# Optimization experiments

Measured on AMD Instinct MI355X. Metric: run time of the kernel, lower is better.

## Reference

```python
import jax, jax.numpy as jnp
import numpy as np

N_NODES = 50000
E_TRAIN = 800000
E_POS = 200000
E_NEG = 200000
F_IN = 128


def gcn_conv(x, W, b, src, dst, n):
    """PyG-style GCNConv: add self-loops, symmetric deg^{-1/2} norm, linear, scatter-add."""
    loop = jnp.arange(n, dtype=src.dtype)
    s = jnp.concatenate([src, loop])  # [E+N]
    d = jnp.concatenate([dst, loop])
    deg = jax.ops.segment_sum(jnp.ones(d.shape, dtype=x.dtype), d, num_segments=n)
    dis = jax.lax.rsqrt(jnp.maximum(deg, 1.0))  # deg >= 1 due to self-loops
    norm = dis[s] * dis[d]  # [E+N]
    h = x @ W  # [N, out]
    msg = h[s] * norm[:, None]  # gather + per-edge scale
    return jax.ops.segment_sum(msg, d, num_segments=n) + b


def reference(x, train_pos_edge_index, pos_edge_index, neg_edge_index, W1, b1, W2, b2, W3, b3):
    src, dst = train_pos_edge_index[0], train_pos_edge_index[1]
    h = jax.nn.relu(gcn_conv(x, W1, b1, src, dst, N_NODES))
    h = jax.nn.relu(gcn_conv(h, W2, b2, src, dst, N_NODES))
    h = gcn_conv(h, W3, b3, src, dst, N_NODES)
    te = jnp.concatenate([pos_edge_index, neg_edge_index], axis=-1)  # [2, E_pos+E_neg]
    x_j = h[te[0]]
    x_i = h[te[1]]
    return jnp.einsum('ef,ef->e', x_i, x_j)


def setup_inputs() -> dict:
    key = jax.random.key(0)
    ks = jax.random.split(key, 10)
    glorot = lambda k, fi, fo: jax.random.normal(k, (fi, fo), dtype=jnp.float32) * np.float32(np.sqrt(2.0 / (fi + fo)))
    return {
        'x': jax.random.normal(ks[0], (N_NODES, F_IN), dtype=jnp.float32),
        'train_pos_edge_index': jax.random.randint(ks[1], (2, E_TRAIN), 0, N_NODES, dtype=jnp.int32),
        'pos_edge_index': jax.random.randint(ks[2], (2, E_POS), 0, N_NODES, dtype=jnp.int32),
        'neg_edge_index': jax.random.randint(ks[3], (2, E_NEG), 0, N_NODES, dtype=jnp.int32),
        'W1': glorot(ks[4], F_IN, 256), 'b1': jnp.zeros((256,), jnp.float32),
        'W2': glorot(ks[5], 256, 128), 'b2': jnp.zeros((128,), jnp.float32),
        'W3': glorot(ks[6], 128, 64), 'b3': jnp.zeros((64,), jnp.float32),
    }
```

## Files before the change

### kernel.cpp

```cpp
#include <hip/hip_runtime.h>
#include <math.h>

#define N_NODES 50000
#define E_TRAIN 800000
#define E_POS 200000
#define E_NEG 200000

#define NBUCK 196
#define BSTRIDE 5120
#define PSTRIDE 9216
#define PARTA_BLOCKS 196


__device__ inline void split_bf16(float f, short& h, short& l) {
    unsigned u = __float_as_uint(f);
    h = (short)(u >> 16);
    float rem = f - __uint_as_float(u & 0xFFFF0000u);
    l = (short)(__float_as_uint(rem) >> 16);
}

__device__ inline unsigned short f2bf_rne(float f) {
    unsigned u = __float_as_uint(f);
    unsigned r = u + 0x7FFFu + ((u >> 16) & 1u);
    return (unsigned short)(r >> 16);
}

__device__ inline float bf2f(unsigned short h) {
    return __uint_as_float(((unsigned)h) << 16);
}

#define WTOT (128 * 256 + 256 * 128 + 128 * 64)


__global__ void partA_prep_kernel(
        const int* __restrict__ src, const int* __restrict__ dst,
        int* __restrict__ gcount, unsigned int* __restrict__ temp, int e,
        const float* __restrict__ W1, short* __restrict__ W1h, short* __restrict__ W1l,
        const float* __restrict__ W2, short* __restrict__ W2h, short* __restrict__ W2l,
        const float* __restrict__ W3, short* __restrict__ W3h, short* __restrict__ W3l,
        const float* __restrict__ x, unsigned short* __restrict__ xb, int n4) {
    __shared__ int hist[NBUCK];
    __shared__ int base[NBUCK];
    __shared__ int lcur[NBUCK];
    int tid = threadIdx.x;
    if (blockIdx.x < PARTA_BLOCKS) {
        for (int i = tid; i < NBUCK; i += 256) hist[i] = 0;
        __syncthreads();
        int start = blockIdx.x * 4096;
        int stop = min(start + 4096, e);
        for (int i = start + tid; i < stop; i += 256)
            atomicAdd(&hist[dst[i] >> 8], 1);
        __syncthreads();
        for (int i = tid; i < NBUCK; i += 256) {
            base[i] = atomicAdd(&gcount[i], hist[i]);
            lcur[i] = 0;
        }
        __syncthreads();
        for (int i = start + tid; i < stop; i += 256) {
            int d = dst[i];
            int b = d >> 8;
            int off = atomicAdd(&lcur[b], 1);
            temp[(size_t)b * BSTRIDE + base[b] + off] = ((unsigned)src[i] << 8) | (unsigned)(d & 255);
        }
    } else {
        int i = (blockIdx.x - PARTA_BLOCKS) * 256 + tid;
        if (i < WTOT) {
            const float* W; short *Wh, *Wl; int K, N;
            if (i < 128 * 256) { W = W1; Wh = W1h; Wl = W1l; K = 128; N = 256; }
            else if (i < 128 * 256 + 256 * 128) { i -= 128 * 256; W = W2; Wh = W2h; Wl = W2l; K = 256; N = 128; }
            else { i -= 128 * 256 + 256 * 128; W = W3; Wh = W3h; Wl = W3l; K = 128; N = 64; }
            int k = i / N, n = i - k * N;
            short h, l;
            split_bf16(W[i], h, l);
            Wh[(size_t)n * K + k] = h;
            Wl[(size_t)n * K + k] = l;
        } else {
            int j = i - WTOT;
            if (j < n4) {
                float4 v = ((const float4*)x)[j];
                ushort4 o;
                o.x = f2bf_rne(v.x); o.y = f2bf_rne(v.y);
                o.z = f2bf_rne(v.z); o.w = f2bf_rne(v.w);
                ((ushort4*)xb)[j] = o;
            }
        }
    }
}


__global__ void partB_kernel(const unsigned int* __restrict__ temp,
                             const int* __restrict__ gcount,
                             float* __restrict__ dis, int* __restrict__ offs, int* __restrict__ ends,
                             unsigned short* __restrict__ csr) {
    __shared__ int cnt[256];
    __shared__ int loc[256];
    __shared__ int cursor[256];
    int b = blockIdx.x;
    int t = threadIdx.x;
    int total = gcount[b];
    size_t tbase = (size_t)b * BSTRIDE;
    cnt[t] = 0;
    __syncthreads();
    for (int i = t; i < total; i += 256)
        atomicAdd(&cnt[temp[tbase + i] & 255], 1);
    __syncthreads();
    int c = cnt[t];
    int pc = (c + 15) & ~15;
    loc[t] = pc;
    __syncthreads();
    for (int d = 1; d < 256; d <<= 1) {
        int u = 0;
        if (t >= d) u = loc[t - d];
        __syncthreads();
        if (t >= d) loc[t] += u;
        __syncthreads();
    }
    int excl = loc[t] - pc;
    int node = b * 256 + t;
    int gstart = b * PSTRIDE + excl;
    if (node < N_NODES) {
        dis[node] = 1.0f / sqrtf((float)(c + 1));
        offs[node] = gstart;
        ends[node] = gstart + pc;
    }
    cursor[t] = gstart;
    __syncthreads();
    for (int i = t; i < total; i += 256) {
        unsigned v = temp[tbase + i];
        int pos = atomicAdd(&cursor[v & 255], 1);
        csr[pos] = (unsigned short)(v >> 8);
    }
    __syncthreads();
    for (int j = c; j < pc; j++)
        csr[gstart + j] = 0xFFFFu;
}

__global__ void wdis_kernel(unsigned short* __restrict__ csr,
                            const float* __restrict__ dis,
                            float* __restrict__ wdis, int n) {
    int i = blockIdx.x * blockDim.x + threadIdx.x;
    if (i < n) {
        unsigned short s = csr[i];
        if (s == 0xFFFFu) { csr[i] = 0; wdis[i] = 0.f; }
        else wdis[i] = dis[s];
    }
}


typedef short bf16x8 __attribute__((ext_vector_type(8)));
typedef float f32x4 __attribute__((ext_vector_type(4)));

template<int BN, bool BR, bool OBF>
__global__ __launch_bounds__(512) void gemm_fulln_kernel(
        const float* __restrict__ A,
        const short* __restrict__ Bth, const short* __restrict__ Btl,
        const float* __restrict__ bias, float* __restrict__ C,
        unsigned short* __restrict__ Cb,
        int M, int K) {
    constexpr int NI = BN / 16;
    constexpr int BCH = BN * 4;
    constexpr int BP = (BCH + 511) / 512;
    constexpr size_t BSZ = (size_t)2 * BN * 40 * 2;
    constexpr size_t TSZ = (size_t)8 * 16 * 68 * 4;
    __shared__ __align__(16) char smem[BSZ > TSZ ? BSZ : TSZ];
    short* Bhi = (short*)smem;
    short* Blo = (short*)(smem + (size_t)BN * 40 * 2);
    float* tr  = (float*)smem;

    int tid = threadIdx.x;
    int lane = tid & 63;
    int wv = tid >> 6;
    int brow = blockIdx.x * 128;
    int m_lane = lane & 15;
    int kgrp = lane >> 4;

    int myrow = brow + wv * 16 + m_lane;
    if (myrow >= M) myrow = M - 1;
    const float* Ap = &A[(size_t)myrow * K + kgrp * 8];

    f32x4 acc[NI];
    #pragma unroll
    for (int i = 0; i < NI; i++) acc[i] = (f32x4){0.f, 0.f, 0.f, 0.f};

    int4 bhReg[BP], blReg[BP];
    float4 aN0, aN1, aC0, aC1;

    auto loadB = [&](int k0) {
        #pragma unroll
        for (int p = 0; p < BP; p++) {
            int idx = p * 512 + tid;
            if (idx < BCH) {
                int col = idx >> 2;
                int kc = idx & 3;
                size_t o = (size_t)col * K + k0 + kc * 8;
                bhReg[p] = *(const int4*)&Bth[o];
                blReg[p] = *(const int4*)&Btl[o];
            }
        }
    };
    auto loadA = [&](int k0) {
        aN0 = *(const float4*)&Ap[k0];
        aN1 = *(const float4*)&Ap[k0 + 4];
    };

    loadB(0); loadA(0);

    for (int k0 = 0; k0 < K; k0 += 32) {
        aC0 = aN0; aC1 = aN1;
        #pragma unroll
        for (int p = 0; p < BP; p++) {
            int idx = p * 512 + tid;
            if (idx < BCH) {
                int col = idx >> 2;
                int kc = idx & 3;
                *(int4*)&Bhi[col * 40 + kc * 8] = bhReg[p];
                *(int4*)&Blo[col * 40 + kc * 8] = blReg[p];
            }
        }
        __syncthreads();

        if (k0 + 32 < K) { loadB(k0 + 32); loadA(k0 + 32); }

        bf16x8 ah, al;
        {
            short h, l;
            split_bf16(aC0.x, h, l); ah[0] = h; al[0] = l;
            split_bf16(aC0.y, h, l); ah[1] = h; al[1] = l;
            split_bf16(aC0.z, h, l); ah[2] = h; al[2] = l;
            split_bf16(aC0.w, h, l); ah[3] = h; al[3] = l;
            split_bf16(aC1.x, h, l); ah[4] = h; al[4] = l;
            split_bf16(aC1.y, h, l); ah[5] = h; al[5] = l;
            split_bf16(aC1.z, h, l); ah[6] = h; al[6] = l;
            split_bf16(aC1.w, h, l); ah[7] = h; al[7] = l;
        }
        #pragma unroll
        for (int ni = 0; ni < NI; ni++) {
            int boff = (ni * 16 + m_lane) * 40 + kgrp * 8;
            bf16x8 bh = *(const bf16x8*)&Bhi[boff];
            bf16x8 bl = *(const bf16x8*)&Blo[boff];
            acc[ni] = __builtin_amdgcn_mfma_f32_16x16x32_bf16(ah, bh, acc[ni], 0, 0, 0);
            acc[ni] = __builtin_amdgcn_mfma_f32_16x16x32_bf16(al, bh, acc[ni], 0, 0, 0);
            acc[ni] = __builtin_amdgcn_mfma_f32_16x16x32_bf16(ah, bl, acc[ni], 0, 0, 0);
        }
        __syncthreads();
    }

    #pragma unroll
    for (int c = 0; c < NI / 4; c++) {
        #pragma unroll
        for (int q = 0; q < 4; q++) {
            int ni = c * 4 + q;
            float bb = 0.f;
            if (BR) bb = bias[ni * 16 + m_lane];
            #pragma unroll
            for (int reg = 0; reg < 4; reg++) {
                float v = acc[ni][reg];
                if (BR) v = fmaxf(v + bb, 0.f);
                tr[wv * 1088 + (kgrp * 4 + reg) * 68 + q * 16 + m_lane] = v;
            }
        }
        #pragma unroll
        for (int j = 0; j < 4; j++) {
            int r = (lane >> 4) + j * 4;
            int g = lane & 15;
            float4 v = *(const float4*)&tr[wv * 1088 + r * 68 + g * 4];
            int row = brow + wv * 16 + r;
            if (row < M) {
                if (OBF) {
                    ushort4 o;
                    o.x = f2bf_rne(v.x); o.y = f2bf_rne(v.y);
                    o.z = f2bf_rne(v.z); o.w = f2bf_rne(v.w);
                    *(ushort4*)&Cb[(size_t)row * BN + c * 64 + g * 4] = o;
                } else {
                    *(float4*)&C[(size_t)row * BN + c * 64 + g * 4] = v;
                }
            }
        }
    }
}


#define AGG_WAVES 12800
#define AGG_BLOCKS (AGG_WAVES / 4)

template<int F, bool RELU, bool BIAS>
__global__ void aggregate_bf16_kernel(const unsigned short* __restrict__ xb,
                                      float* __restrict__ out,
                                      const float* __restrict__ dis,
                                      const int* __restrict__ starts,
                                      const int* __restrict__ ends,
                                      const unsigned short* __restrict__ csr_src,
                                      const float* __restrict__ wdis,
                                      const float* __restrict__ bias,
                                      int n) {
    int wid = (blockIdx.x * blockDim.x + threadIdx.x) >> 6;
    int lane = threadIdx.x & 63;
    constexpr int VPT = F / 64;

    for (int v = wid; v < n; v += AGG_WAVES) {
        float dv = dis[v];
        float acc[VPT];
        if constexpr (VPT == 2) {
            ushort2 sv = *(const ushort2*)&xb[(size_t)v * F + lane * 2];
            acc[0] = bf2f(sv.x) * dv * dv;
            acc[1] = bf2f(sv.y) * dv * dv;
        } else {
            acc[0] = bf2f(xb[(size_t)v * F + lane]) * dv * dv;
        }
        int s = __builtin_amdgcn_readfirstlane(starts[v]);
        int e = __builtin_amdgcn_readfirstlane(ends[v]);
        for (int p = s; p < e; p += 16) {
            int4 c0 = *(const int4*)&csr_src[p];
            int4 c1 = *(const int4*)&csr_src[p + 8];
            float4 w0 = *(const float4*)&wdis[p];
            float4 w1 = *(const float4*)&wdis[p + 4];
            float4 w2 = *(const float4*)&wdis[p + 8];
            float4 w3 = *(const float4*)&wdis[p + 12];
            int u[16];
            u[0] = (unsigned)c0.x & 0xFFFF; u[1] = (unsigned)c0.x >> 16;
            u[2] = (unsigned)c0.y & 0xFFFF; u[3] = (unsigned)c0.y >> 16;
            u[4] = (unsigned)c0.z & 0xFFFF; u[5] = (unsigned)c0.z >> 16;
            u[6] = (unsigned)c0.w & 0xFFFF; u[7] = (unsigned)c0.w >> 16;
            u[8] = (unsigned)c1.x & 0xFFFF; u[9] = (unsigned)c1.x >> 16;
            u[10] = (unsigned)c1.y & 0xFFFF; u[11] = (unsigned)c1.y >> 16;
            u[12] = (unsigned)c1.z & 0xFFFF; u[13] = (unsigned)c1.z >> 16;
            u[14] = (unsigned)c1.w & 0xFFFF; u[15] = (unsigned)c1.w >> 16;
            float w[16];
            w[0] = w0.x * dv; w[1] = w0.y * dv; w[2] = w0.z * dv; w[3] = w0.w * dv;
            w[4] = w1.x * dv; w[5] = w1.y * dv; w[6] = w1.z * dv; w[7] = w1.w * dv;
            w[8] = w2.x * dv; w[9] = w2.y * dv; w[10] = w2.z * dv; w[11] = w2.w * dv;
            w[12] = w3.x * dv; w[13] = w3.y * dv; w[14] = w3.z * dv; w[15] = w3.w * dv;
            if constexpr (VPT == 2) {
                ushort2 g[16];
                #pragma unroll
                for (int q = 0; q < 16; q++)
                    g[q] = *(const ushort2*)&xb[(size_t)u[q] * F + lane * 2];
                #pragma unroll
                for (int q = 0; q < 16; q++) {
                    acc[0] += bf2f(g[q].x) * w[q];
                    acc[1] += bf2f(g[q].y) * w[q];
                }
            } else {
                unsigned short g[16];
                #pragma unroll
                for (int q = 0; q < 16; q++)
                    g[q] = xb[(size_t)u[q] * F + lane];
                #pragma unroll
                for (int q = 0; q < 16; q++) acc[0] += bf2f(g[q]) * w[q];
            }
        }
        float* o = &out[(size_t)v * F + lane * VPT];
        #pragma unroll
        for (int i = 0; i < VPT; i++) {
            float r = acc[i];
            if (BIAS) r += bias[lane * VPT + i];
            if (RELU) r = fmaxf(r, 0.f);
            o[i] = r;
        }
    }
}


__global__ void dot_kernel(const float* __restrict__ h,
                           const int* __restrict__ pos, const int* __restrict__ neg,
                           float* __restrict__ out) {
    int gw = (blockIdx.x * blockDim.x + threadIdx.x) >> 6;
    int lane = threadIdx.x & 63;
    int sub = lane >> 4;
    int pl = lane & 15;
    int e = gw * 4 + sub;
    if (e >= E_POS + E_NEG) return;
    int i0, i1;
    if (e < E_POS) { i0 = pos[e]; i1 = pos[E_POS + e]; }
    else { int t = e - E_POS; i0 = neg[t]; i1 = neg[E_NEG + t]; }
    float4 a = *(const float4*)&h[(size_t)i0 * 64 + pl * 4];
    float4 b = *(const float4*)&h[(size_t)i1 * 64 + pl * 4];
    float v = a.x * b.x + a.y * b.y + a.z * b.z + a.w * b.w;
    v += __shfl_xor(v, 1, 64);
    v += __shfl_xor(v, 2, 64);
    v += __shfl_xor(v, 4, 64);
    v += __shfl_xor(v, 8, 64);
    if (pl == 0) out[e] = v;
}


extern "C" void kernel_launch(void* const* d_in, const int* in_sizes, int n_in,
                              void* d_out, int out_size, void* d_ws, size_t ws_size,
                              hipStream_t stream) {
    const float* x  = (const float*)d_in[0];
    const int* tei  = (const int*)d_in[1];
    const int* pos  = (const int*)d_in[2];
    const int* neg  = (const int*)d_in[3];
    const float* W1 = (const float*)d_in[4];
    const float* b1 = (const float*)d_in[5];
    const float* W2 = (const float*)d_in[6];
    const float* b2 = (const float*)d_in[7];
    const float* W3 = (const float*)d_in[8];
    const float* b3 = (const float*)d_in[9];
    float* out = (float*)d_out;

    const int* src = tei;
    const int* dst = tei + E_TRAIN;

    char* ws = (char*)d_ws;
    size_t off = 0;
    auto alloc = [&](size_t bytes) -> void* {
        void* p = ws + off;
        off = (off + bytes + 255) & ~(size_t)255;
        return p;
    };
    unsigned short* xb   = (unsigned short*)alloc((size_t)N_NODES * 128 * 2);
    float* aggX          = (float*)alloc((size_t)N_NODES * 128 * 4);
    float* h1            = (float*)alloc((size_t)N_NODES * 256 * 4);
    unsigned short* xw2b = (unsigned short*)alloc((size_t)N_NODES * 128 * 2);
    float* h2            = (float*)alloc((size_t)N_NODES * 128 * 4);
    unsigned short* xw3b = (unsigned short*)alloc((size_t)N_NODES * 64 * 2);
    float* h3            = (float*)alloc((size_t)N_NODES * 64 * 4);
    float* dis  = (float*)alloc(N_NODES * 4);
    int* offs   = (int*)alloc(N_NODES * 4);
    int* ends   = (int*)alloc(N_NODES * 4);
    int* gcount = (int*)alloc(NBUCK * 4);
    unsigned int* temp  = (unsigned int*)alloc((size_t)NBUCK * BSTRIDE * 4);
    unsigned short* csr = (unsigned short*)alloc((size_t)NBUCK * PSTRIDE * 2);
    float* wdis         = (float*)alloc((size_t)NBUCK * PSTRIDE * 4);
    short* Wt1h = (short*)alloc((size_t)128 * 256 * 2);
    short* Wt1l = (short*)alloc((size_t)128 * 256 * 2);
    short* Wt2h = (short*)alloc((size_t)256 * 128 * 2);
    short* Wt2l = (short*)alloc((size_t)256 * 128 * 2);
    short* Wt3h = (short*)alloc((size_t)128 * 64 * 2);
    short* Wt3l = (short*)alloc((size_t)128 * 64 * 2);
    (void)ws_size; (void)n_in; (void)in_sizes; (void)out_size;

    const int n4 = N_NODES * 128 / 4;

    hipMemsetAsync(gcount, 0, NBUCK * 4, stream);
    {
        int prep_blocks = (WTOT + n4 + 255) / 256;
        partA_prep_kernel<<<PARTA_BLOCKS + prep_blocks, 256, 0, stream>>>(
            src, dst, gcount, temp, E_TRAIN,
            W1, Wt1h, Wt1l, W2, Wt2h, Wt2l, W3, Wt3h, Wt3l, x, xb, n4);
    }
    partB_kernel<<<NBUCK, 256, 0, stream>>>(temp, gcount, dis, offs, ends, csr);
    {
        int ncsr = NBUCK * PSTRIDE;
        wdis_kernel<<<(ncsr + 255) / 256, 256, 0, stream>>>(csr, dis, wdis, ncsr);
    }

    const int GB = (N_NODES + 127) / 128;

    aggregate_bf16_kernel<128, false, false><<<AGG_BLOCKS, 256, 0, stream>>>(
        xb, aggX, dis, offs, ends, csr, wdis, nullptr, N_NODES);
    gemm_fulln_kernel<256, true, false><<<GB, 512, 0, stream>>>(
        aggX, Wt1h, Wt1l, b1, h1, nullptr, N_NODES, 128);

    gemm_fulln_kernel<128, false, true><<<GB, 512, 0, stream>>>(
        h1, Wt2h, Wt2l, nullptr, nullptr, xw2b, N_NODES, 256);
    aggregate_bf16_kernel<128, true, true><<<AGG_BLOCKS, 256, 0, stream>>>(
        xw2b, h2, dis, offs, ends, csr, wdis, b2, N_NODES);

    gemm_fulln_kernel<64, false, true><<<GB, 512, 0, stream>>>(
        h2, Wt3h, Wt3l, nullptr, nullptr, xw3b, N_NODES, 128);
    aggregate_bf16_kernel<64, false, true><<<AGG_BLOCKS, 256, 0, stream>>>(
        xw3b, h3, dis, offs, ends, csr, wdis, b3, N_NODES);

    const int DOT_WAVES = (E_POS + E_NEG + 3) / 4;
    dot_kernel<<<(DOT_WAVES + 3) / 4, 256, 0, stream>>>(h3, pos, neg, out);
}
```

Measured before the change: 293.6 us.

## Store intermediates as pre-split bf16 hi/lo pairs and shrink CSR padding

Aggregation and GEMM outputs are now written as separate bf16 hi and lo arrays, so the next GEMM loads bf16x8 vectors directly instead of reading fp32 and splitting in its inner loop. Per-node CSR padding drops from a multiple of 16 to a multiple of 8, and the aggregation loop processes 8 edges per step, which cuts padded gather work. The destination deg^-1/2 factor is applied once at the end rather than on every edge weight. Memory traffic for the hi/lo arrays is the same as for fp32, and the shorter edge loop exposes less load parallelism per iteration.

```diff
diff --git a/kernel.cpp b/kernel.cpp
--- a/kernel.cpp
+++ b/kernel.cpp
@@ -8,7 +8,7 @@
 
 #define NBUCK 196
 #define BSTRIDE 5120
-#define PSTRIDE 9216
+#define PSTRIDE 6912
 #define PARTA_BLOCKS 196
 
 
@@ -105,7 +105,7 @@
         atomicAdd(&cnt[temp[tbase + i] & 255], 1);
     __syncthreads();
     int c = cnt[t];
-    int pc = (c + 15) & ~15;
+    int pc = (c + 7) & ~7;
     loc[t] = pc;
     __syncthreads();
     for (int d = 1; d < 256; d <<= 1) {
@@ -152,9 +152,10 @@
 
 template<int BN, bool BR, bool OBF>
 __global__ __launch_bounds__(512) void gemm_fulln_kernel(
-        const float* __restrict__ A,
+        const short* __restrict__ Ah, const short* __restrict__ Al,
         const short* __restrict__ Bth, const short* __restrict__ Btl,
-        const float* __restrict__ bias, float* __restrict__ C,
+        const float* __restrict__ bias,
+        short* __restrict__ Ch, short* __restrict__ Cl,
         unsigned short* __restrict__ Cb,
         int M, int K) {
     constexpr int NI = BN / 16;
@@ -176,14 +177,15 @@
 
     int myrow = brow + wv * 16 + m_lane;
     if (myrow >= M) myrow = M - 1;
-    const float* Ap = &A[(size_t)myrow * K + kgrp * 8];
+    const short* Aph = &Ah[(size_t)myrow * K + kgrp * 8];
+    const short* Apl = &Al[(size_t)myrow * K + kgrp * 8];
 
     f32x4 acc[NI];
     #pragma unroll
     for (int i = 0; i < NI; i++) acc[i] = (f32x4){0.f, 0.f, 0.f, 0.f};
 
     int4 bhReg[BP], blReg[BP];
-    float4 aN0, aN1, aC0, aC1;
+    bf16x8 ahN, alN, ahC, alC;
 
     auto loadB = [&](int k0) {
         #pragma unroll
@@ -199,14 +201,14 @@
         }
     };
     auto loadA = [&](int k0) {
-        aN0 = *(const float4*)&Ap[k0];
-        aN1 = *(const float4*)&Ap[k0 + 4];
+        ahN = *(const bf16x8*)&Aph[k0];
+        alN = *(const bf16x8*)&Apl[k0];
     };
 
     loadB(0); loadA(0);
 
     for (int k0 = 0; k0 < K; k0 += 32) {
-        aC0 = aN0; aC1 = aN1;
+        ahC = ahN; alC = alN;
         #pragma unroll
         for (int p = 0; p < BP; p++) {
             int idx = p * 512 + tid;
@@ -221,26 +223,14 @@
 
         if (k0 + 32 < K) { loadB(k0 + 32); loadA(k0 + 32); }
 
-        bf16x8 ah, al;
-        {
-            short h, l;
-            split_bf16(aC0.x, h, l); ah[0] = h; al[0] = l;
-            split_bf16(aC0.y, h, l); ah[1] = h; al[1] = l;
-            split_bf16(aC0.z, h, l); ah[2] = h; al[2] = l;
-            split_bf16(aC0.w, h, l); ah[3] = h; al[3] = l;
-            split_bf16(aC1.x, h, l); ah[4] = h; al[4] = l;
-            split_bf16(aC1.y, h, l); ah[5] = h; al[5] = l;
-            split_bf16(aC1.z, h, l); ah[6] = h; al[6] = l;
-            split_bf16(aC1.w, h, l); ah[7] = h; al[7] = l;
-        }
         #pragma unroll
         for (int ni = 0; ni < NI; ni++) {
             int boff = (ni * 16 + m_lane) * 40 + kgrp * 8;
             bf16x8 bh = *(const bf16x8*)&Bhi[boff];
             bf16x8 bl = *(const bf16x8*)&Blo[boff];
-            acc[ni] = __builtin_amdgcn_mfma_f32_16x16x32_bf16(ah, bh, acc[ni], 0, 0, 0);
-            acc[ni] = __builtin_amdgcn_mfma_f32_16x16x32_bf16(al, bh, acc[ni], 0, 0, 0);
-            acc[ni] = __builtin_amdgcn_mfma_f32_16x16x32_bf16(ah, bl, acc[ni], 0, 0, 0);
+            acc[ni] = __builtin_amdgcn_mfma_f32_16x16x32_bf16(ahC, bh, acc[ni], 0, 0, 0);
+            acc[ni] = __builtin_amdgcn_mfma_f32_16x16x32_bf16(alC, bh, acc[ni], 0, 0, 0);
+            acc[ni] = __builtin_amdgcn_mfma_f32_16x16x32_bf16(ahC, bl, acc[ni], 0, 0, 0);
         }
         __syncthreads();
     }
@@ -272,7 +262,14 @@
                     o.z = f2bf_rne(v.z); o.w = f2bf_rne(v.w);
                     *(ushort4*)&Cb[(size_t)row * BN + c * 64 + g * 4] = o;
                 } else {
-                    *(float4*)&C[(size_t)row * BN + c * 64 + g * 4] = v;
+                    short4 oh, ol;
+                    short h, l;
+                    split_bf16(v.x, h, l); oh.x = h; ol.x = l;
+                    split_bf16(v.y, h, l); oh.y = h; ol.y = l;
+                    split_bf16(v.z, h, l); oh.z = h; ol.z = l;
+                    split_bf16(v.w, h, l); oh.w = h; ol.w = l;
+                    *(short4*)&Ch[(size_t)row * BN + c * 64 + g * 4] = oh;
+                    *(short4*)&Cl[(size_t)row * BN + c * 64 + g * 4] = ol;
                 }
             }
         }
@@ -283,9 +280,11 @@
 #define AGG_WAVES 12800
 #define AGG_BLOCKS (AGG_WAVES / 4)
 
-template<int F, bool RELU, bool BIAS>
+template<int F, bool RELU, bool BIAS, int OUTM>
 __global__ void aggregate_bf16_kernel(const unsigned short* __restrict__ xb,
-                                      float* __restrict__ out,
+                                      short* __restrict__ outh,
+                                      short* __restrict__ outl,
+                                      float* __restrict__ outf,
                                       const float* __restrict__ dis,
                                       const int* __restrict__ starts,
                                       const int* __restrict__ ends,
@@ -302,60 +301,74 @@
         float acc[VPT];
         if constexpr (VPT == 2) {
             ushort2 sv = *(const ushort2*)&xb[(size_t)v * F + lane * 2];
-            acc[0] = bf2f(sv.x) * dv * dv;
-            acc[1] = bf2f(sv.y) * dv * dv;
+            acc[0] = bf2f(sv.x) * dv;
+            acc[1] = bf2f(sv.y) * dv;
         } else {
-            acc[0] = bf2f(xb[(size_t)v * F + lane]) * dv * dv;
+            acc[0] = bf2f(xb[(size_t)v * F + lane]) * dv;
         }
         int s = __builtin_amdgcn_readfirstlane(starts[v]);
         int e = __builtin_amdgcn_readfirstlane(ends[v]);
-        for (int p = s; p < e; p += 16) {
+        for (int p = s; p < e; p += 8) {
             int4 c0 = *(const int4*)&csr_src[p];
-            int4 c1 = *(const int4*)&csr_src[p + 8];
             float4 w0 = *(const float4*)&wdis[p];
             float4 w1 = *(const float4*)&wdis[p + 4];
-            float4 w2 = *(const float4*)&wdis[p + 8];
-            float4 w3 = *(const float4*)&wdis[p + 12];
-            int u[16];
+            int u[8];
             u[0] = (unsigned)c0.x & 0xFFFF; u[1] = (unsigned)c0.x >> 16;
             u[2] = (unsigned)c0.y & 0xFFFF; u[3] = (unsigned)c0.y >> 16;
             u[4] = (unsigned)c0.z & 0xFFFF; u[5] = (unsigned)c0.z >> 16;
             u[6] = (unsigned)c0.w & 0xFFFF; u[7] = (unsigned)c0.w >> 16;
-            u[8] = (unsigned)c1.x & 0xFFFF; u[9] = (unsigned)c1.x >> 16;
-            u[10] = (unsigned)c1.y & 0xFFFF; u[11] = (unsigned)c1.y >> 16;
-            u[12] = (unsigned)c1.z & 0xFFFF; u[13] = (unsigned)c1.z >> 16;
-            u[14] = (unsigned)c1.w & 0xFFFF; u[15] = (unsigned)c1.w >> 16;
-            float w[16];
-            w[0] = w0.x * dv; w[1] = w0.y * dv; w[2] = w0.z * dv; w[3] = w0.w * dv;
-            w[4] = w1.x * dv; w[5] = w1.y * dv; w[6] = w1.z * dv; w[7] = w1.w * dv;
-            w[8] = w2.x * dv; w[9] = w2.y * dv; w[10] = w2.z * dv; w[11] = w2.w * dv;
-            w[12] = w3.x * dv; w[13] = w3.y * dv; w[14] = w3.z * dv; w[15] = w3.w * dv;
+            float w[8];
+            w[0] = w0.x; w[1] = w0.y; w[2] = w0.z; w[3] = w0.w;
+            w[4] = w1.x; w[5] = w1.y; w[6] = w1.z; w[7] = w1.w;
             if constexpr (VPT == 2) {
-                ushort2 g[16];
+                ushort2 g[8];
                 #pragma unroll
-                for (int q = 0; q < 16; q++)
+                for (int q = 0; q < 8; q++)
                     g[q] = *(const ushort2*)&xb[(size_t)u[q] * F + lane * 2];
                 #pragma unroll
-                for (int q = 0; q < 16; q++) {
+                for (int q = 0; q < 8; q++) {
                     acc[0] += bf2f(g[q].x) * w[q];
                     acc[1] += bf2f(g[q].y) * w[q];
                 }
             } else {
-                unsigned short g[16];
+                unsigned short g[8];
                 #pragma unroll
-                for (int q = 0; q < 16; q++)
+                for (int q = 0; q < 8; q++)
                     g[q] = xb[(size_t)u[q] * F + lane];
                 #pragma unroll
-                for (int q = 0; q < 16; q++) acc[0] += bf2f(g[q]) * w[q];
-            }
-        }
-        float* o = &out[(size_t)v * F + lane * VPT];
-        #pragma unroll
-        for (int i = 0; i < VPT; i++) {
-            float r = acc[i];
-            if (BIAS) r += bias[lane * VPT + i];
-            if (RELU) r = fmaxf(r, 0.f);
-            o[i] = r;
+                for (int q = 0; q < 8; q++) acc[0] += bf2f(g[q]) * w[q];
+            }
+        }
+        size_t base = (size_t)v * F + lane * VPT;
+        if constexpr (OUTM == 1) {
+            #pragma unroll
+            for (int i = 0; i < VPT; i++) {
+                float r = acc[i] * dv;
+                if (BIAS) r += bias[lane * VPT + i];
+                if (RELU) r = fmaxf(r, 0.f);
+                outf[base + i] = r;
+            }
+        } else {
+            if constexpr (VPT == 2) {
+                float r0 = acc[0] * dv, r1 = acc[1] * dv;
+                if (BIAS) { r0 += bias[lane * 2]; r1 += bias[lane * 2 + 1]; }
+                if (RELU) { r0 = fmaxf(r0, 0.f); r1 = fmaxf(r1, 0.f); }
+                short h0, l0, h1, l1;
+                split_bf16(r0, h0, l0);
+                split_bf16(r1, h1, l1);
+                short2 oh; oh.x = h0; oh.y = h1;
+                short2 ol; ol.x = l0; ol.y = l1;
+                *(short2*)&outh[base] = oh;
+                *(short2*)&outl[base] = ol;
+            } else {
+                float r = acc[0] * dv;
+                if (BIAS) r += bias[lane];
+                if (RELU) r = fmaxf(r, 0.f);
+                short h, l;
+                split_bf16(r, h, l);
+                outh[base] = h;
+                outl[base] = l;
+            }
         }
     }
 }
@@ -409,13 +422,16 @@
         off = (off + bytes + 255) & ~(size_t)255;
         return p;
     };
-    unsigned short* xb   = (unsigned short*)alloc((size_t)N_NODES * 128 * 2);
-    float* aggX          = (float*)alloc((size_t)N_NODES * 128 * 4);
-    float* h1            = (float*)alloc((size_t)N_NODES * 256 * 4);
+    unsigned short* xb = (unsigned short*)alloc((size_t)N_NODES * 128 * 2);
+    short* aggXh       = (short*)alloc((size_t)N_NODES * 128 * 2);
+    short* aggXl       = (short*)alloc((size_t)N_NODES * 128 * 2);
+    short* h1h         = (short*)alloc((size_t)N_NODES * 256 * 2);
+    short* h1l         = (short*)alloc((size_t)N_NODES * 256 * 2);
     unsigned short* xw2b = (unsigned short*)alloc((size_t)N_NODES * 128 * 2);
-    float* h2            = (float*)alloc((size_t)N_NODES * 128 * 4);
+    short* h2h         = (short*)alloc((size_t)N_NODES * 128 * 2);
+    short* h2l         = (short*)alloc((size_t)N_NODES * 128 * 2);
     unsigned short* xw3b = (unsigned short*)alloc((size_t)N_NODES * 64 * 2);
-    float* h3            = (float*)alloc((size_t)N_NODES * 64 * 4);
+    float* h3          = (float*)alloc((size_t)N_NODES * 64 * 4);
     float* dis  = (float*)alloc(N_NODES * 4);
     int* offs   = (int*)alloc(N_NODES * 4);
     int* ends   = (int*)alloc(N_NODES * 4);
@@ -448,20 +464,20 @@
 
     const int GB = (N_NODES + 127) / 128;
 
-    aggregate_bf16_kernel<128, false, false><<<AGG_BLOCKS, 256, 0, stream>>>(
-        xb, aggX, dis, offs, ends, csr, wdis, nullptr, N_NODES);
+    aggregate_bf16_kernel<128, false, false, 0><<<AGG_BLOCKS, 256, 0, stream>>>(
+        xb, aggXh, aggXl, nullptr, dis, offs, ends, csr, wdis, nullptr, N_NODES);
     gemm_fulln_kernel<256, true, false><<<GB, 512, 0, stream>>>(
-        aggX, Wt1h, Wt1l, b1, h1, nullptr, N_NODES, 128);
+        aggXh, aggXl, Wt1h, Wt1l, b1, h1h, h1l, nullptr, N_NODES, 128);
 
     gemm_fulln_kernel<128, false, true><<<GB, 512, 0, stream>>>(
-        h1, Wt2h, Wt2l, nullptr, nullptr, xw2b, N_NODES, 256);
-    aggregate_bf16_kernel<128, true, true><<<AGG_BLOCKS, 256, 0, stream>>>(
-        xw2b, h2, dis, offs, ends, csr, wdis, b2, N_NODES);
+        h1h, h1l, Wt2h, Wt2l, nullptr, nullptr, nullptr, xw2b, N_NODES, 256);
+    aggregate_bf16_kernel<128, true, true, 0><<<AGG_BLOCKS, 256, 0, stream>>>(
+        xw2b, h2h, h2l, nullptr, dis, offs, ends, csr, wdis, b2, N_NODES);
 
     gemm_fulln_kernel<64, false, true><<<GB, 512, 0, stream>>>(
-        h2, Wt3h, Wt3l, nullptr, nullptr, xw3b, N_NODES, 128);
-    aggregate_bf16_kernel<64, false, true><<<AGG_BLOCKS, 256, 0, stream>>>(
-        xw3b, h3, dis, offs, ends, csr, wdis, b3, N_NODES);
+        h2h, h2l, Wt3h, Wt3l, nullptr, nullptr, nullptr, xw3b, N_NODES, 128);
+    aggregate_bf16_kernel<64, false, true, 1><<<AGG_BLOCKS, 256, 0, stream>>>(
+        xw3b, nullptr, nullptr, h3, dis, offs, ends, csr, wdis, b3, N_NODES);
 
     const int DOT_WAVES = (E_POS + E_NEG + 3) / 4;
     dot_kernel<<<(DOT_WAVES + 3) / 4, 256, 0, stream>>>(h3, pos, neg, out);
```

After: 297.1 us (median of 2 runs). About the same (+1.2%).
